# Kernel tuning notes

Measured on AMD Instinct MI355X. Metric: run time of the kernel, lower is better.

Reference implementation:

```python
import jax, jax.numpy as jnp
import numpy as np

B, T, D, H, O = 512, 512, 256, 200, 1


def setup_inputs() -> dict:
    key = jax.random.key(0)
    ks = jax.random.split(key, 7)
    s = 1.0 / np.sqrt(H)  # PyTorch LSTM init scale
    x = jax.random.normal(ks[0], (B, T, D), dtype=jnp.float32)
    W_ih = jax.random.uniform(ks[1], (4 * H, D), jnp.float32, -s, s)
    W_hh = jax.random.uniform(ks[2], (4 * H, H), jnp.float32, -s, s)
    b_ih = jax.random.uniform(ks[3], (4 * H,), jnp.float32, -s, s)
    b_hh = jax.random.uniform(ks[4], (4 * H,), jnp.float32, -s, s)
    so = 1.0 / np.sqrt(H * T)
    W_out = jax.random.uniform(ks[5], (O, H * T), jnp.float32, -so, so)
    b_out = jax.random.uniform(ks[6], (O,), jnp.float32, -so, so)
    return {"input_seq": x, "W_ih": W_ih, "W_hh": W_hh, "b_ih": b_ih,
            "b_hh": b_hh, "W_out": W_out, "b_out": b_out}


def _lstm(x, W_ih, W_hh, b_ih, b_hh):
    # Precompute input contribution for all timesteps: [B,T,4H] -> [T,B,4H]
    pre = jnp.einsum('btd,gd->btg', x, W_ih) + b_ih + b_hh
    pre = jnp.transpose(pre, (1, 0, 2))
    h0 = jnp.zeros((x.shape[0], H), x.dtype)
    c0 = jnp.zeros((x.shape[0], H), x.dtype)

    def step(carry, pt):
        h, c = carry
        gates = pt + h @ W_hh.T  # [B,4H]
        i, f, g, o = jnp.split(gates, 4, axis=-1)  # PyTorch gate order i,f,g,o
        i = jax.nn.sigmoid(i)
        f = jax.nn.sigmoid(f)
        g = jnp.tanh(g)
        o = jax.nn.sigmoid(o)
        c_new = f * c + i * g
        h_new = o * jnp.tanh(c_new)
        return (h_new, c_new), h_new

    _, outs = jax.lax.scan(step, (h0, c0), pre)  # outs: [T,B,H]
    return jnp.transpose(outs, (1, 0, 2))  # [B,T,H]


def reference(input_seq, W_ih, W_hh, b_ih, b_hh, W_out, b_out):
    all_outs = _lstm(input_seq, W_ih, W_hh, b_ih, b_hh)  # [B,T,H]
    flat = all_outs.reshape(all_outs.shape[0], -1)  # [B, T*H]
    return flat @ W_out.T + b_out  # [B, O]
```

## Files before the change

### kernel.cpp

```cpp
#include <hip/hip_runtime.h>
#include <hip/hip_bf16.h>

#define B_SZ 512
#define T_SZ 512
#define D_SZ 256
#define H_SZ 200
#define G4   800
#define NSUB 50
#define GST8 808
#define GDUMP (2*GST8)
#define HTS  232
#define BS   8

typedef __attribute__((ext_vector_type(8))) short short8;
typedef __attribute__((ext_vector_type(4))) short short4v;
typedef __attribute__((ext_vector_type(4))) float f32x4;

__device__ __forceinline__ unsigned short f2bf(float x) {
    unsigned u = __builtin_bit_cast(unsigned, x);
    unsigned r = (u + 0x7FFFu + ((u >> 16) & 1u)) >> 16;
    return (unsigned short)r;
}
__device__ __forceinline__ float sigm(float v) { return 1.f / (1.f + __expf(-v)); }

__device__ __forceinline__ void gl_lds16(const void* g, void* l) {
    __builtin_amdgcn_global_load_lds(
        (const __attribute__((address_space(1))) unsigned int*)g,
        (__attribute__((address_space(3))) unsigned int*)l, 16, 0, 0);
}

__global__ __launch_bounds__(256)
void cvt_bf16(const float* __restrict__ src, unsigned short* __restrict__ dst, int n4)
{
    int i = blockIdx.x * 256 + threadIdx.x;
    const int stride = gridDim.x * 256;
    for (; i < n4; i += stride) {
        float4 v = ((const float4*)src)[i];
        unsigned a = (unsigned)f2bf(v.x) | ((unsigned)f2bf(v.y) << 16);
        unsigned b = (unsigned)f2bf(v.z) | ((unsigned)f2bf(v.w) << 16);
        ((uint2*)dst)[i] = make_uint2(a, b);
    }
}

__global__ __launch_bounds__(256)
void pre_gemm(const unsigned short* __restrict__ xbf,
              const unsigned short* __restrict__ wbf,
              const float* __restrict__ bih, const float* __restrict__ bhh,
              unsigned short* __restrict__ pre, int t0)
{
    const int tt = blockIdx.x;
    const int t  = t0 + tt;
    const int b0 = blockIdx.y * 64;
    const int g0 = blockIdx.z * 256;

    __shared__ unsigned short Al[256 * 32];
    __shared__ unsigned short Bl[64 * 32];

    const int tid  = threadIdx.x;
    const int w    = tid >> 6;
    const int lane = tid & 63;
    const int col  = lane & 15, q = lane >> 4;

    f32x4 acc[4][4];
    #pragma unroll
    for (int i = 0; i < 4; ++i)
        #pragma unroll
        for (int j = 0; j < 4; ++j) acc[i][j] = (f32x4)0.f;

    const int arow = w * 64 + (lane >> 2);
    const int akoff = (lane & 3) * 8;
    const int brow = b0 + w * 16 + (lane >> 2);

    for (int kc = 0; kc < 8; ++kc) {
        const int d0 = kc * 32;
        if (kc) __syncthreads();
        #pragma unroll
        for (int j = 0; j < 4; ++j) {
            int g = g0 + arow + j * 16;
            if (g > G4 - 1) g = G4 - 1;
            gl_lds16(wbf + (size_t)g * D_SZ + d0 + akoff,
                     (void*)(Al + (w * 64 + j * 16) * 32));
        }
        gl_lds16(xbf + ((size_t)brow * T_SZ + t) * D_SZ + d0 + akoff,
                 (void*)(Bl + (w * 16) * 32));
        __syncthreads();

        short8 af[4], bv[4];
        #pragma unroll
        for (int s = 0; s < 4; ++s)
            af[s] = *(const short8*)&Al[(w * 64 + s * 16 + col) * 32 + q * 8];
        #pragma unroll
        for (int s = 0; s < 4; ++s)
            bv[s] = *(const short8*)&Bl[(s * 16 + col) * 32 + q * 8];
        #pragma unroll
        for (int gs = 0; gs < 4; ++gs)
            #pragma unroll
            for (int bs = 0; bs < 4; ++bs)
                acc[gs][bs] = __builtin_amdgcn_mfma_f32_16x16x32_bf16(af[gs], bv[bs], acc[gs][bs], 0, 0, 0);
    }

    #pragma unroll
    for (int gs = 0; gs < 4; ++gs) {
        const int S = blockIdx.z * 16 + w * 4 + gs;
        if (S < NSUB) {
            const int gq = S * 16 + q * 4;
            const float4 bi = *(const float4*)&bih[gq];
            const float4 bh = *(const float4*)&bhh[gq];
            #pragma unroll
            for (int bs = 0; bs < 4; ++bs) {
                f32x4 a = acc[gs][bs];
                unsigned lo = (unsigned)f2bf(a[0] + bi.x + bh.x) |
                              ((unsigned)f2bf(a[1] + bi.y + bh.y) << 16);
                unsigned hi = (unsigned)f2bf(a[2] + bi.z + bh.z) |
                              ((unsigned)f2bf(a[3] + bi.w + bh.w) << 16);
                const size_t idx = (((size_t)tt * NSUB + S) * 4 + q) * 512 + (b0 + bs * 16 + col);
                ((uint2*)pre)[idx] = make_uint2(lo, hi);
            }
        }
    }
}

__global__ __launch_bounds__(512, 2)
void lstm_rec(const unsigned short* __restrict__ pre,
              const float* __restrict__ Whh,
              const float* __restrict__ Wout,
              const float* __restrict__ bout,
              float* __restrict__ state,
              float* __restrict__ out,
              int t0, int C_T)
{
    const int bk = blockIdx.x;
    const int cidx = (bk >> 3) + (bk & 7) * 32;
    const int b0 = cidx * 2;

    const int tid = threadIdx.x, lane = tid & 63, wv = tid >> 6;
    const int col = lane & 15, q = lane >> 4;

    __shared__ __align__(16) unsigned short preS[2 * BS * 1600];
    __shared__ __align__(16) float gates[2 * GST8 + 256];
    __shared__ __align__(16) short hT[3 * HTS];
    __shared__ float redbuf[8];

    const int tbase = (wv < 2) ? wv * 7 : 14 + (wv - 2) * 6;

    int gaddr[7], pofs[7], tjv[7];
    #pragma unroll
    for (int j = 0; j < 7; ++j) {
        const int tr = tbase + j;
        const int tj = tr > 49 ? 49 : tr;
        tjv[j] = tj;
        const bool valid = (tr <= 49) && (col < 2);
        gaddr[j] = valid ? (col * GST8 + tj * 16 + q * 4) : (GDUMP + lane * 4);
        pofs[j]  = (tj * 4 + q) * 8 + (col & 1) * 4;
    }

    short8 aw[7][6];
#if __has_builtin(__builtin_amdgcn_mfma_f32_16x16x16bf16_1k)
    short4v aw6[7];
#else
    short8 aw6[7];
#endif
    #pragma unroll
    for (int j = 0; j < 7; ++j) {
        const int g = tjv[j] * 16 + col;
        const float* wr = Whh + (size_t)g * H_SZ;
        #pragma unroll
        for (int kc = 0; kc < 6; ++kc) {
            const int k = kc * 32 + q * 8;
            float4 f0 = *(const float4*)(wr + k);
            float4 f1 = *(const float4*)(wr + k + 4);
            short8 s;
            s[0] = (short)f2bf(f0.x); s[1] = (short)f2bf(f0.y);
            s[2] = (short)f2bf(f0.z); s[3] = (short)f2bf(f0.w);
            s[4] = (short)f2bf(f1.x); s[5] = (short)f2bf(f1.y);
            s[6] = (short)f2bf(f1.z); s[7] = (short)f2bf(f1.w);
            aw[j][kc] = s;
        }
#if __has_builtin(__builtin_amdgcn_mfma_f32_16x16x16bf16_1k)
        short4v t4 = (short4v)0;
        if (q < 2) {
            float4 f = *(const float4*)(wr + 192 + q * 4);
            t4[0] = (short)f2bf(f.x); t4[1] = (short)f2bf(f.y);
            t4[2] = (short)f2bf(f.z); t4[3] = (short)f2bf(f.w);
        }
        aw6[j] = t4;
#else
        short8 t8 = (short8)0;
        if (q == 0) {
            float4 f0 = *(const float4*)(wr + 192);
            float4 f1 = *(const float4*)(wr + 196);
            t8[0] = (short)f2bf(f0.x); t8[1] = (short)f2bf(f0.y);
            t8[2] = (short)f2bf(f0.z); t8[3] = (short)f2bf(f0.w);
            t8[4] = (short)f2bf(f1.x); t8[5] = (short)f2bf(f1.y);
            t8[6] = (short)f2bf(f1.z); t8[7] = (short)f2bf(f1.w);
        }
        aw6[j] = t8;
#endif
    }

    float* h_st  = state;
    float* c_st  = state + (size_t)B_SZ * H_SZ;
    float* oa_st = state + (size_t)2 * B_SZ * H_SZ;

    for (int i = tid; i < 3 * HTS; i += 512) {
        const int r = i / HTS, k = i - r * HTS;
        short v = 0;
        if (t0 > 0 && r < 2 && k < H_SZ) v = (short)f2bf(h_st[(size_t)(b0 + r) * H_SZ + k]);
        hT[i] = v;
    }

    const int n_ew = tid >> 8;
    const int h_ew = tid & 255;
    const bool ewv = (h_ew < H_SZ);
    float c_v = 0.f, oa_v = 0.f, wpf0 = 0.f, wpf1 = 0.f;
    if (ewv) {
        wpf0 = Wout[(size_t)t0 * H_SZ + h_ew];
        const int t1 = (t0 + 1 < T_SZ) ? t0 + 1 : T_SZ - 1;
        wpf1 = Wout[(size_t)t1 * H_SZ + h_ew];
        if (t0 > 0) {
            c_v  = c_st [(size_t)(b0 + n_ew) * H_SZ + h_ew];
            oa_v = oa_st[(size_t)(b0 + n_ew) * H_SZ + h_ew];
        }
    }

    const int nblk = C_T / BS;
    const char* preb = (const char*)pre;

    {
        const char* src = preb + ((size_t)wv * 200) * 4096 + (size_t)b0 * 8;
        unsigned short* dst = preS + (0 * BS + wv) * 1600;
        gl_lds16(src + (size_t)lane * 4096,         dst);
        gl_lds16(src + (size_t)(lane + 64) * 4096,  dst + 512);
        gl_lds16(src + (size_t)(lane + 128) * 4096, dst + 1024);
        gl_lds16(src + (size_t)(lane + 136) * 4096, dst + 1088);
    }
    __syncthreads();

    const short* hrow = hT + (col < 2 ? col : 2) * HTS;

    for (int blk = 0; blk < nblk; ++blk) {
        const int bn = blk & 1;
        {
            const int nb = (blk + 1 < nblk) ? blk + 1 : blk;
            const char* src = preb + ((size_t)(nb * BS + wv) * 200) * 4096 + (size_t)b0 * 8;
            unsigned short* dst = preS + ((bn ^ 1) * BS + wv) * 1600;
            gl_lds16(src + (size_t)lane * 4096,         dst);
            gl_lds16(src + (size_t)(lane + 64) * 4096,  dst + 512);
            gl_lds16(src + (size_t)(lane + 128) * 4096, dst + 1024);
            gl_lds16(src + (size_t)(lane + 136) * 4096, dst + 1088);
        }
        const unsigned short* psb = preS + bn * (BS * 1600);

        for (int s = 0; s < BS; ++s) {
            const int tc = blk * BS + s;
            const unsigned short* ps = psb + s * 1600;

            f32x4 acc[7];
            #pragma unroll
            for (int j = 0; j < 7; ++j) {
                const uint2 p = *(const uint2*)(ps + pofs[j]);
                f32x4 a;
                a[0] = __builtin_bit_cast(float, p.x << 16);
                a[1] = __builtin_bit_cast(float, p.x & 0xFFFF0000u);
                a[2] = __builtin_bit_cast(float, p.y << 16);
                a[3] = __builtin_bit_cast(float, p.y & 0xFFFF0000u);
                acc[j] = a;
            }
            #pragma unroll
            for (int kc = 0; kc < 6; ++kc) {
                const short8 bf = *(const short8*)(hrow + kc * 32 + q * 8);
                #pragma unroll
                for (int j = 0; j < 7; ++j)
                    acc[j] = __builtin_amdgcn_mfma_f32_16x16x32_bf16(aw[j][kc], bf, acc[j], 0, 0, 0);
            }
#if __has_builtin(__builtin_amdgcn_mfma_f32_16x16x16bf16_1k)
            {
                const short4v bt = *(const short4v*)(hrow + 192 + q * 4);
                #pragma unroll
                for (int j = 0; j < 7; ++j)
                    acc[j] = __builtin_amdgcn_mfma_f32_16x16x16bf16_1k(aw6[j], bt, acc[j], 0, 0, 0);
            }
#else
            {
                const short8 bt = *(const short8*)(hrow + 192 + q * 8);
                #pragma unroll
                for (int j = 0; j < 7; ++j)
                    acc[j] = __builtin_amdgcn_mfma_f32_16x16x32_bf16(aw6[j], bt, acc[j], 0, 0, 0);
            }
#endif
            #pragma unroll
            for (int j = 0; j < 7; ++j)
                *(f32x4*)&gates[gaddr[j]] = acc[j];
            __syncthreads();

            if (ewv) {
                const int gb = n_ew * GST8 + h_ew;
                const float gi = sigm(gates[gb]);
                const float gf = sigm(gates[gb + 200]);
                const float gg = 2.f * sigm(2.f * gates[gb + 400]) - 1.f;
                const float go = sigm(gates[gb + 600]);
                const float cn = gf * c_v + gi * gg;
                c_v = cn;
                const float hv = go * (2.f * sigm(2.f * cn) - 1.f);
                oa_v += hv * wpf0;
                wpf0 = wpf1;
                const int tn = (t0 + tc + 2 < T_SZ) ? t0 + tc + 2 : T_SZ - 1;
                wpf1 = Wout[(size_t)tn * H_SZ + h_ew];
                hT[n_ew * HTS + h_ew] = (short)f2bf(hv);
                if (t0 + C_T < T_SZ && tc == C_T - 1)
                    h_st[(size_t)(b0 + n_ew) * H_SZ + h_ew] = hv;
            }
            __syncthreads();
        }
    }

    if (t0 + C_T >= T_SZ) {
        float v = oa_v;
        #pragma unroll
        for (int off = 32; off; off >>= 1) v += __shfl_down(v, off);
        if (lane == 0) redbuf[wv] = v;
        __syncthreads();
        if (tid < 2)
            out[b0 + tid] = redbuf[tid * 4] + redbuf[tid * 4 + 1] +
                            redbuf[tid * 4 + 2] + redbuf[tid * 4 + 3] + bout[0];
    } else if (ewv) {
        c_st [(size_t)(b0 + n_ew) * H_SZ + h_ew] = c_v;
        oa_st[(size_t)(b0 + n_ew) * H_SZ + h_ew] = oa_v;
    }
}

extern "C" void kernel_launch(void* const* d_in, const int* in_sizes, int n_in,
                              void* d_out, int out_size, void* d_ws, size_t ws_size,
                              hipStream_t stream)
{
    const float* x    = (const float*)d_in[0];
    const float* Wih  = (const float*)d_in[1];
    const float* Whh  = (const float*)d_in[2];
    const float* bih  = (const float*)d_in[3];
    const float* bhh  = (const float*)d_in[4];
    const float* Wout = (const float*)d_in[5];
    const float* bout = (const float*)d_in[6];
    float* out = (float*)d_out;

    char* ws = (char*)d_ws;
    float* state = (float*)ws;
    size_t off = (size_t)3 * B_SZ * H_SZ * sizeof(float);
    unsigned short* xbf = (unsigned short*)(ws + off);
    off += (size_t)B_SZ * T_SZ * D_SZ * 2;
    unsigned short* wbf = (unsigned short*)(ws + off);
    off += (size_t)G4 * D_SZ * 2;
    unsigned short* pre = (unsigned short*)(ws + off);

    const size_t per_t = (size_t)NSUB * 4 * 512 * 4 * 2;
    int ct = 512;
    while (ct > BS && off + (size_t)ct * per_t > ws_size) ct >>= 1;

    cvt_bf16<<<dim3(2048), dim3(256), 0, stream>>>(x, xbf, B_SZ * T_SZ * D_SZ / 4);
    cvt_bf16<<<dim3(64),   dim3(256), 0, stream>>>(Wih, wbf, G4 * D_SZ / 4);

    for (int t0 = 0; t0 < T_SZ; t0 += ct) {
        pre_gemm<<<dim3(ct, 8, 4), dim3(256), 0, stream>>>(
            xbf, wbf, bih, bhh, pre, t0);
        lstm_rec<<<dim3(256), dim3(512), 0, stream>>>(
            pre, Whh, Wout, bout, state, out, t0, ct);
    }
}
```

Measured before the change: 1.872 ms.

## Interleave gate rows so each lane computes cell update directly from MFMA accumulators

Permutes the W_ih/W_hh rows and the fused bias so that the four gates (i,f,g,o) of one hidden unit land in the same MFMA accumulator lane. The elementwise LSTM update then runs straight from registers, which removes the LDS gates buffer and one of the two per-step barriers. It also double-buffers h in LDS and streams W_out rows into LDS through async global-to-LDS loads. The cost is extra prep kernels, a runtime select across the accumulators, and the elementwise work is now spread over more lanes with some left idle.

```diff
diff --git a/kernel.cpp b/kernel.cpp
--- a/kernel.cpp
+++ b/kernel.cpp
@@ -7,10 +7,8 @@
 #define H_SZ 200
 #define G4   800
 #define NSUB 50
-#define GST8 808
-#define GDUMP (2*GST8)
-#define HTS  232
 #define BS   8
+#define WROW 800
 
 typedef __attribute__((ext_vector_type(8))) short short8;
 typedef __attribute__((ext_vector_type(4))) short short4v;
@@ -43,9 +41,36 @@
 }
 
 __global__ __launch_bounds__(256)
+void cvt_w_perm(const float* __restrict__ Wih, unsigned short* __restrict__ dst)
+{
+    int i = blockIdx.x * 256 + threadIdx.x;
+    if (i >= G4 * (D_SZ / 4)) return;
+    const int r = i >> 6, ch = i & 63;
+    const int p = (r & 3) * H_SZ + (r >> 2);
+    float4 v = ((const float4*)(Wih + (size_t)p * D_SZ))[ch];
+    unsigned a = (unsigned)f2bf(v.x) | ((unsigned)f2bf(v.y) << 16);
+    unsigned b = (unsigned)f2bf(v.z) | ((unsigned)f2bf(v.w) << 16);
+    ((uint2*)dst)[i] = make_uint2(a, b);
+}
+
+__global__ __launch_bounds__(256)
+void prep(const float* __restrict__ bih, const float* __restrict__ bhh,
+          const float* __restrict__ Wout, float* __restrict__ bsum,
+          float* __restrict__ wpad)
+{
+    const int i = blockIdx.x * 256 + threadIdx.x;
+    if (i < G4) {
+        const int p = (i & 3) * H_SZ + (i >> 2);
+        bsum[i] = bih[p] + bhh[p];
+    }
+    if (i < T_SZ * H_SZ + 256)
+        wpad[i] = (i < T_SZ * H_SZ) ? Wout[i] : 0.f;
+}
+
+__global__ __launch_bounds__(256)
 void pre_gemm(const unsigned short* __restrict__ xbf,
               const unsigned short* __restrict__ wbf,
-              const float* __restrict__ bih, const float* __restrict__ bhh,
+              const float* __restrict__ bs,
               unsigned short* __restrict__ pre, int t0)
 {
     const int tt = blockIdx.x;
@@ -95,8 +120,8 @@
         #pragma unroll
         for (int gs = 0; gs < 4; ++gs)
             #pragma unroll
-            for (int bs = 0; bs < 4; ++bs)
-                acc[gs][bs] = __builtin_amdgcn_mfma_f32_16x16x32_bf16(af[gs], bv[bs], acc[gs][bs], 0, 0, 0);
+            for (int bsi = 0; bsi < 4; ++bsi)
+                acc[gs][bsi] = __builtin_amdgcn_mfma_f32_16x16x32_bf16(af[gs], bv[bsi], acc[gs][bsi], 0, 0, 0);
     }
 
     #pragma unroll
@@ -104,16 +129,15 @@
         const int S = blockIdx.z * 16 + w * 4 + gs;
         if (S < NSUB) {
             const int gq = S * 16 + q * 4;
-            const float4 bi = *(const float4*)&bih[gq];
-            const float4 bh = *(const float4*)&bhh[gq];
-            #pragma unroll
-            for (int bs = 0; bs < 4; ++bs) {
-                f32x4 a = acc[gs][bs];
-                unsigned lo = (unsigned)f2bf(a[0] + bi.x + bh.x) |
-                              ((unsigned)f2bf(a[1] + bi.y + bh.y) << 16);
-                unsigned hi = (unsigned)f2bf(a[2] + bi.z + bh.z) |
-                              ((unsigned)f2bf(a[3] + bi.w + bh.w) << 16);
-                const size_t idx = (((size_t)tt * NSUB + S) * 4 + q) * 512 + (b0 + bs * 16 + col);
+            const float4 bi = *(const float4*)&bs[gq];
+            #pragma unroll
+            for (int bsi = 0; bsi < 4; ++bsi) {
+                f32x4 a = acc[gs][bsi];
+                unsigned lo = (unsigned)f2bf(a[0] + bi.x) |
+                              ((unsigned)f2bf(a[1] + bi.y) << 16);
+                unsigned hi = (unsigned)f2bf(a[2] + bi.z) |
+                              ((unsigned)f2bf(a[3] + bi.w) << 16);
+                const size_t idx = (((size_t)tt * NSUB + S) * 4 + q) * 512 + (b0 + bsi * 16 + col);
                 ((uint2*)pre)[idx] = make_uint2(lo, hi);
             }
         }
@@ -123,7 +147,7 @@
 __global__ __launch_bounds__(512, 2)
 void lstm_rec(const unsigned short* __restrict__ pre,
               const float* __restrict__ Whh,
-              const float* __restrict__ Wout,
+              const float* __restrict__ wpad,
               const float* __restrict__ bout,
               float* __restrict__ state,
               float* __restrict__ out,
@@ -137,22 +161,27 @@
     const int col = lane & 15, q = lane >> 4;
 
     __shared__ __align__(16) unsigned short preS[2 * BS * 1600];
-    __shared__ __align__(16) float gates[2 * GST8 + 256];
-    __shared__ __align__(16) short hT[3 * HTS];
-    __shared__ float redbuf[8];
+    __shared__ __align__(16) short hT[1600];
+    __shared__ __align__(16) float woutS[2 * 256];
+    __shared__ float redbuf[16];
 
     const int tbase = (wv < 2) ? wv * 7 : 14 + (wv - 2) * 6;
 
-    int gaddr[7], pofs[7], tjv[7];
+    int pofs[7], tjv[7];
     #pragma unroll
     for (int j = 0; j < 7; ++j) {
         const int tr = tbase + j;
         const int tj = tr > 49 ? 49 : tr;
         tjv[j] = tj;
-        const bool valid = (tr <= 49) && (col < 2);
-        gaddr[j] = valid ? (col * GST8 + tj * 16 + q * 4) : (GDUMP + lane * 4);
-        pofs[j]  = (tj * 4 + q) * 8 + (col & 1) * 4;
-    }
+        pofs[j] = (tj * 4 + q) * 8 + (col >> 3) * 4;
+    }
+    const int c7 = col & 7;
+    const int jsel = (c7 < 7) ? c7 : 6;
+    const bool valid = (wv < 2) ? (c7 < 7) : (c7 < 6);
+    const int bsel = col >> 3;
+    const int usel = tjv[jsel] * 4 + q;
+    const int hw_base = valid ? (bsel * 256 + usel) : (1024 + lane);
+    const int rbase = bsel * 256;
 
     short8 aw[7][6];
 #if __has_builtin(__builtin_amdgcn_mfma_f32_16x16x16bf16_1k)
@@ -162,8 +191,8 @@
 #endif
     #pragma unroll
     for (int j = 0; j < 7; ++j) {
-        const int g = tjv[j] * 16 + col;
-        const float* wr = Whh + (size_t)g * H_SZ;
+        const int gp = tjv[j] * 16 + col;
+        const float* wr = Whh + (size_t)((gp & 3) * H_SZ + (gp >> 2)) * H_SZ;
         #pragma unroll
         for (int kc = 0; kc < 6; ++kc) {
             const int k = kc * 32 + q * 8;
@@ -202,25 +231,19 @@
     float* c_st  = state + (size_t)B_SZ * H_SZ;
     float* oa_st = state + (size_t)2 * B_SZ * H_SZ;
 
-    for (int i = tid; i < 3 * HTS; i += 512) {
-        const int r = i / HTS, k = i - r * HTS;
+    for (int i = tid; i < 1600; i += 512) {
         short v = 0;
-        if (t0 > 0 && r < 2 && k < H_SZ) v = (short)f2bf(h_st[(size_t)(b0 + r) * H_SZ + k]);
+        if (t0 > 0 && i < 512) {
+            const int r = i >> 8, u = i & 255;
+            if (u < H_SZ) v = (short)f2bf(h_st[(size_t)(b0 + r) * H_SZ + u]);
+        }
         hT[i] = v;
     }
 
-    const int n_ew = tid >> 8;
-    const int h_ew = tid & 255;
-    const bool ewv = (h_ew < H_SZ);
-    float c_v = 0.f, oa_v = 0.f, wpf0 = 0.f, wpf1 = 0.f;
-    if (ewv) {
-        wpf0 = Wout[(size_t)t0 * H_SZ + h_ew];
-        const int t1 = (t0 + 1 < T_SZ) ? t0 + 1 : T_SZ - 1;
-        wpf1 = Wout[(size_t)t1 * H_SZ + h_ew];
-        if (t0 > 0) {
-            c_v  = c_st [(size_t)(b0 + n_ew) * H_SZ + h_ew];
-            oa_v = oa_st[(size_t)(b0 + n_ew) * H_SZ + h_ew];
-        }
+    float c_v = 0.f, oa_v = 0.f;
+    if (t0 > 0 && valid) {
+        c_v  = c_st [(size_t)(b0 + bsel) * H_SZ + usel];
+        oa_v = oa_st[(size_t)(b0 + bsel) * H_SZ + usel];
     }
 
     const int nblk = C_T / BS;
@@ -234,9 +257,9 @@
         gl_lds16(src + (size_t)(lane + 128) * 4096, dst + 1024);
         gl_lds16(src + (size_t)(lane + 136) * 4096, dst + 1088);
     }
+    if (wv == 7)
+        gl_lds16((const char*)wpad + (size_t)t0 * WROW + lane * 16, (void*)woutS);
     __syncthreads();
-
-    const short* hrow = hT + (col < 2 ? col : 2) * HTS;
 
     for (int blk = 0; blk < nblk; ++blk) {
         const int bn = blk & 1;
@@ -255,6 +278,14 @@
             const int tc = blk * BS + s;
             const unsigned short* ps = psb + s * 1600;
 
+            if (wv == 7) {
+                int tn = t0 + tc + 1; if (tn > T_SZ - 1) tn = T_SZ - 1;
+                gl_lds16((const char*)wpad + (size_t)tn * WROW + lane * 16,
+                         (void*)(woutS + ((tc + 1) & 1) * 256));
+            }
+
+            const short* hrow = hT + ((tc & 1) << 9) + rbase;
+
             f32x4 acc[7];
             #pragma unroll
             for (int j = 0; j < 7; ++j) {
@@ -288,44 +319,45 @@
                     acc[j] = __builtin_amdgcn_mfma_f32_16x16x32_bf16(aw6[j], bt, acc[j], 0, 0, 0);
             }
 #endif
-            #pragma unroll
-            for (int j = 0; j < 7; ++j)
-                *(f32x4*)&gates[gaddr[j]] = acc[j];
+            f32x4 sel = acc[0];
+            #pragma unroll
+            for (int j = 1; j < 7; ++j)
+                if (jsel == j) sel = acc[j];
+
+            const float gi = sigm(sel[0]);
+            const float gf = sigm(sel[1]);
+            const float gg = 2.f * sigm(2.f * sel[2]) - 1.f;
+            const float go = sigm(sel[3]);
+            const float cn = gf * c_v + gi * gg;
+            c_v = cn;
+            const float hv = go * (2.f * sigm(2.f * cn) - 1.f);
+            oa_v += hv * woutS[(tc & 1) * 256 + usel];
+            hT[hw_base + (((tc + 1) & 1) << 9)] = (short)f2bf(hv);
+            if (t0 + C_T < T_SZ && tc == C_T - 1 && valid)
+                h_st[(size_t)(b0 + bsel) * H_SZ + usel] = hv;
             __syncthreads();
-
-            if (ewv) {
-                const int gb = n_ew * GST8 + h_ew;
-                const float gi = sigm(gates[gb]);
-                const float gf = sigm(gates[gb + 200]);
-                const float gg = 2.f * sigm(2.f * gates[gb + 400]) - 1.f;
-                const float go = sigm(gates[gb + 600]);
-                const float cn = gf * c_v + gi * gg;
-                c_v = cn;
-                const float hv = go * (2.f * sigm(2.f * cn) - 1.f);
-                oa_v += hv * wpf0;
-                wpf0 = wpf1;
-                const int tn = (t0 + tc + 2 < T_SZ) ? t0 + tc + 2 : T_SZ - 1;
-                wpf1 = Wout[(size_t)tn * H_SZ + h_ew];
-                hT[n_ew * HTS + h_ew] = (short)f2bf(hv);
-                if (t0 + C_T < T_SZ && tc == C_T - 1)
-                    h_st[(size_t)(b0 + n_ew) * H_SZ + h_ew] = hv;
-            }
-            __syncthreads();
         }
     }
 
     if (t0 + C_T >= T_SZ) {
-        float v = oa_v;
-        #pragma unroll
-        for (int off = 32; off; off >>= 1) v += __shfl_down(v, off);
-        if (lane == 0) redbuf[wv] = v;
+        float v = valid ? oa_v : 0.f;
+        v += __shfl_xor(v, 1);
+        v += __shfl_xor(v, 2);
+        v += __shfl_xor(v, 4);
+        v += __shfl_xor(v, 16);
+        v += __shfl_xor(v, 32);
+        if (lane == 0) redbuf[wv * 2]     = v;
+        if (lane == 8) redbuf[wv * 2 + 1] = v;
         __syncthreads();
-        if (tid < 2)
-            out[b0 + tid] = redbuf[tid * 4] + redbuf[tid * 4 + 1] +
-                            redbuf[tid * 4 + 2] + redbuf[tid * 4 + 3] + bout[0];
-    } else if (ewv) {
-        c_st [(size_t)(b0 + n_ew) * H_SZ + h_ew] = c_v;
-        oa_st[(size_t)(b0 + n_ew) * H_SZ + h_ew] = oa_v;
+        if (tid < 2) {
+            float r = bout[0];
+            #pragma unroll
+            for (int w = 0; w < 8; ++w) r += redbuf[w * 2 + tid];
+            out[b0 + tid] = r;
+        }
+    } else if (valid) {
+        c_st [(size_t)(b0 + bsel) * H_SZ + usel] = c_v;
+        oa_st[(size_t)(b0 + bsel) * H_SZ + usel] = oa_v;
     }
 }
 
@@ -345,6 +377,10 @@
     char* ws = (char*)d_ws;
     float* state = (float*)ws;
     size_t off = (size_t)3 * B_SZ * H_SZ * sizeof(float);
+    float* bsum = (float*)(ws + off);
+    off += (size_t)G4 * sizeof(float);
+    float* wpad = (float*)(ws + off);
+    off += (size_t)(T_SZ * H_SZ + 256) * sizeof(float);
     unsigned short* xbf = (unsigned short*)(ws + off);
     off += (size_t)B_SZ * T_SZ * D_SZ * 2;
     unsigned short* wbf = (unsigned short*)(ws + off);
@@ -356,12 +392,13 @@
     while (ct > BS && off + (size_t)ct * per_t > ws_size) ct >>= 1;
 
     cvt_bf16<<<dim3(2048), dim3(256), 0, stream>>>(x, xbf, B_SZ * T_SZ * D_SZ / 4);
-    cvt_bf16<<<dim3(64),   dim3(256), 0, stream>>>(Wih, wbf, G4 * D_SZ / 4);
+    cvt_w_perm<<<dim3(200), dim3(256), 0, stream>>>(Wih, wbf);
+    prep<<<dim3(402), dim3(256), 0, stream>>>(bih, bhh, Wout, bsum, wpad);
 
     for (int t0 = 0; t0 < T_SZ; t0 += ct) {
         pre_gemm<<<dim3(ct, 8, 4), dim3(256), 0, stream>>>(
-            xbf, wbf, bih, bhh, pre, t0);
+            xbf, wbf, bsum, pre, t0);
         lstm_rec<<<dim3(256), dim3(512), 0, stream>>>(
-            pre, Whh, Wout, bout, state, out, t0, ct);
-    }
-}
+            pre, Whh, wpad, bout, state, out, t0, ct);
+    }
+}
```

Measured after the change: 1.638 ms. 1.14x faster.
